# Performance work log

Hardware: AMD Instinct MI355X
Metric: run time of the kernel (lower is better)

The kernel has to match this reference:

```python
import jax, jax.numpy as jnp
import numpy as np

B, N, QD = 2, 2048, 1024
CTX_LEN, TCD = 77, 768
NUM_PROMPT, PD = 64, 1024
HEADS, DIM_HEAD = 8, 64
INNER = HEADS * DIM_HEAD  # 512
SCALE = DIM_HEAD ** -0.5


def setup_inputs() -> dict:
    key = jax.random.key(0)
    ks = jax.random.split(key, 10)
    s = lambda *sh: 1.0 / np.sqrt(sh[0])
    return {
        "x": jax.random.normal(ks[0], (B, N, QD), jnp.float32),
        "context": jax.random.normal(ks[1], (B, CTX_LEN, TCD), jnp.float32),
        "prompt": jax.random.normal(ks[2], (1, NUM_PROMPT, PD), jnp.float32),
        "w_prompt": jax.random.normal(ks[3], (PD, TCD), jnp.float32) * s(PD),
        "w_img": jax.random.normal(ks[4], (QD, TCD), jnp.float32) * s(QD),
        "w_q": jax.random.normal(ks[5], (QD, INNER), jnp.float32) * s(QD),
        "w_k": jax.random.normal(ks[6], (TCD, INNER), jnp.float32) * s(TCD),
        "w_v": jax.random.normal(ks[7], (TCD, INNER), jnp.float32) * s(TCD),
        "w_out": jax.random.normal(ks[8], (INNER, QD), jnp.float32) * s(INNER),
        "b_out": jax.random.normal(ks[9], (QD,), jnp.float32) * 0.01,
    }


def reference(x, context, prompt, w_prompt, w_img, w_q, w_k, w_v, w_out, b_out):
    b, n, _ = x.shape
    # q projection
    q = x @ w_q  # [B, N, INNER]
    # build kv context: [text ; projected prompt ; projected image tokens]
    prompt_ctx = jnp.broadcast_to(prompt @ w_prompt, (b, NUM_PROMPT, TCD))
    img_ctx = x @ w_img  # [B, N, TCD]
    ctx = jnp.concatenate([context, prompt_ctx, img_ctx], axis=1)  # [B, J, TCD]
    k = ctx @ w_k
    v = ctx @ w_v
    # split heads: [B, H, L, D]
    split = lambda t: t.reshape(b, t.shape[1], HEADS, DIM_HEAD).transpose(0, 2, 1, 3)
    qh, kh, vh = split(q), split(k), split(v)
    sim = jnp.einsum("bhid,bhjd->bhij", qh, kh) * SCALE
    attn = jax.nn.softmax(sim, axis=-1)
    out = jnp.einsum("bhij,bhjd->bhid", attn, vh)  # [B, H, N, D]
    out = out.transpose(0, 2, 1, 3).reshape(b, n, INNER)
    return out @ w_out + b_out
```

## Files before the change

kernel.cpp:

```cpp
#include <hip/hip_runtime.h>
#include <hip/hip_bf16.h>
#include <math.h>

#define BB 2
#define NN 2048
#define QD 1024
#define CTX_LEN 77
#define TCD 768
#define NUM_PROMPT 64
#define PD 1024
#define HEADS 8
#define DIM_HEAD 64
#define INNER 512
#define JTOT (CTX_LEN + NUM_PROMPT + NN)
#define SCALE 0.125f
#define SCALEL2 (0.125f * 1.44269504088896f)
#define MTOT (BB * NN)
#define JPAD 2240
#define KVPAD 2304
#define NT_J (JPAD / 64)
#define NT_SPLIT 18

typedef unsigned short u16;
typedef unsigned int u32;
typedef __attribute__((ext_vector_type(8))) short bf16x8;
typedef __attribute__((ext_vector_type(4))) float f32x4;

__device__ __forceinline__ u32 pack_split(float f) {
  u32 u = __builtin_bit_cast(u32, f);
  u32 hi = u & 0xffff0000u;
  float lo = f - __builtin_bit_cast(float, hi);
  u32 ul = __builtin_bit_cast(u32, lo);
  return __builtin_amdgcn_perm(ul, u, 0x07060302u);
}
__device__ __forceinline__ void split2(float f, u16& h, u16& l) {
  u32 u = __builtin_bit_cast(u32, f);
  u32 hm = u & 0xffff0000u;
  float lo = f - __builtin_bit_cast(float, hm);
  h = (u16)(u >> 16);
  l = (u16)(__builtin_bit_cast(u32, lo) >> 16);
}
__device__ __forceinline__ u16 rnd_bf16(float f) {
  u32 u = __builtin_bit_cast(u32, f);
  return (u16)((u + 0x7FFF + ((u >> 16) & 1)) >> 16);
}
__device__ __forceinline__ ushort4 pack4r(const float4& f) {
  ushort4 r;
  r.x = rnd_bf16(f.x); r.y = rnd_bf16(f.y);
  r.z = rnd_bf16(f.z); r.w = rnd_bf16(f.w);
  return r;
}

template <int CTRL>
__device__ __forceinline__ float dpp_f(float x) {
  int i = __builtin_bit_cast(int, x);
  i = __builtin_amdgcn_update_dpp(0, i, CTRL, 0xF, 0xF, false);
  return __builtin_bit_cast(float, i);
}

__device__ __forceinline__ void gload16(const u16* g, u32* l) {
  __builtin_amdgcn_global_load_lds(
      (const __attribute__((address_space(1))) u32*)(const void*)g,
      (__attribute__((address_space(3))) u32*)(void*)l, 16, 0, 0);
}

__global__ __launch_bounds__(256) void pack_planes4(
    const float* __restrict__ s0, u16* __restrict__ d0, int n0,
    const float* __restrict__ s1, u16* __restrict__ d1, int n1,
    const float* __restrict__ ctx, u16* __restrict__ ch, int n2,
    u16* __restrict__ zh, int n3) {
  int i = blockIdx.x * 256 + threadIdx.x;
  if (i < n0) {
    ((ushort4*)d0)[i] = pack4r(((const float4*)s0)[i]);
    return;
  }
  i -= n0;
  if (i < n1) {
    ((ushort4*)d1)[i] = pack4r(((const float4*)s1)[i]);
    return;
  }
  i -= n1;
  if (i < n2) {
    ushort4 rr = pack4r(((const float4*)ctx)[i]);
    int c4 = i % (TCD / 4);
    int rb = i / (TCD / 4);
    int r = rb % CTX_LEN, b = rb / CTX_LEN;
    size_t o = ((size_t)b * JTOT + r) * (TCD / 4) + c4;
    ((ushort4*)ch)[o] = rr;
    return;
  }
  i -= n2;
  if (i >= n3) return;
  int c = i & 7;
  int row = i >> 3;
  int d = row & 511;
  int b = row >> 9;
  uint4 z = {0u, 0u, 0u, 0u};
  *(uint4*)&zh[((size_t)b * INNER + d) * KVPAD + 2176 + c * 8] = z;
}

struct TP6 {
  const float* src[6];
  u16* dh[6];
  u16* dl[6];
  int K[6], N[6];
  int blk0[7];
};

__global__ __launch_bounds__(256) void transpose_pack6(TP6 P) {
  __shared__ u32 T[32][33];
  const int bid = blockIdx.x;
  int s = 0;
#pragma unroll
  for (int k = 1; k < 6; ++k) s += (bid >= P.blk0[k]);
  const int rel = bid - P.blk0[s];
  const int N = P.N[s], K = P.K[s];
  const int nbx = N >> 5;
  const int bx = rel % nbx, by = rel / nbx;
  const float* __restrict__ src = P.src[s];
  u16* __restrict__ dh = P.dh[s];
  u16* __restrict__ dl = P.dl[s];
  const int t = threadIdx.x;
  const int k0 = by * 32, n0 = bx * 32;
#pragma unroll
  for (int i = 0; i < 4; ++i) {
    int e = t + i * 256;
    int kr = e >> 5, nc = e & 31;
    T[kr][nc] = pack_split(src[(size_t)(k0 + kr) * N + n0 + nc]);
  }
  __syncthreads();
#pragma unroll
  for (int i = 0; i < 4; ++i) {
    int e = t + i * 256;
    int nr = e >> 5, kc = e & 31;
    u32 w = T[kc][nr];
    size_t idx = (size_t)(n0 + nr) * K + k0 + kc;
    if (dl) {
      dh[idx] = (u16)(w & 0xffff);
      dl[idx] = (u16)(w >> 16);
    } else {
      dh[idx] = (u16)(w & 0xffff);
    }
  }
}

template <int MODE>
__global__ __launch_bounds__(256) void gemm_mfma(
    const u16* __restrict__ Agh, const u16* __restrict__ Agl,
    const u16* __restrict__ Bgh, const u16* __restrict__ Bgl,
    u16* __restrict__ O1h,
    u16* __restrict__ O2h,
    float* __restrict__ Of, const float* __restrict__ bias,
    int M, int K, int Ntot,
    const u16* __restrict__ A2h, const u16* __restrict__ B2h) {
  constexpr bool ONET = (MODE == 1 || MODE == 2);
  constexpr int ALSZ = ONET ? 4 : 2 * 128 * 16;
  constexpr int BLSZ = ONET ? 4 : 2 * 64 * 16;
  __shared__ __align__(16) u32 Ah_s[2][128 * 16];
  __shared__ __align__(16) u32 Al_s[ALSZ];
  __shared__ __align__(16) u32 Bh_s[2][64 * 16];
  __shared__ __align__(16) u32 Bl_s[BLSZ];

  int bxi = blockIdx.x, byi = blockIdx.y;
  {
    const int GX = gridDim.x;
    const int nwg = GX * gridDim.y;
    const int lid = byi * GX + bxi;
    const int qq = nwg >> 3, rr = nwg & 7;
    const int xcd = lid & 7, pos = lid >> 3;
    const int swz = (xcd < rr ? xcd * (qq + 1) : rr * (qq + 1) + (xcd - rr) * qq) + pos;
    bxi = swz % GX; byi = swz / GX;
  }
  const int bm = byi * 128, bn = bxi * 64;

  const bool pband = (MODE == 1) && (bm >= MTOT);
  if (pband && bn >= TCD) return;

  int b2 = 0, jbase = 0;
  if (MODE == 2) { b2 = (byi >= 18); jbase = (byi - b2 * 18) * 128; }

  const int t = threadIdx.x;
  const int w = t >> 6, lane = t & 63;
  const int m16 = lane & 15, quad = lane >> 4;
  const int wm = w >> 1, wn = w & 1;

  const u16* Abh = Agh; const u16* Abl = Agl;
  const u16* Bbh = Bgh; const u16* Bbl = Bgl;
  int rowlim = M - 1;
  int bmA = bm;
  if (pband) { Abh = A2h; Bbh = B2h; rowlim = NUM_PROMPT - 1; bmA = 0; }

  const int acol = (lane & 3) * 8;
  const int ar0 = 32 * w + (lane >> 2);
  const int ar1 = ar0 + 16;
  int ag0, ag1;
  if (MODE == 2) {
    ag0 = b2 * JTOT + min(jbase + ar0, JTOT - 1);
    ag1 = b2 * JTOT + min(jbase + ar1, JTOT - 1);
  } else {
    ag0 = min(bmA + ar0, rowlim);
    ag1 = min(bmA + ar1, rowlim);
  }
  const u16* a0h = Abh + (size_t)ag0 * K + acol;
  const u16* a1h = Abh + (size_t)ag1 * K + acol;
  const u16* a0l = ONET ? nullptr : Abl + (size_t)ag0 * K + acol;
  const u16* a1l = ONET ? nullptr : Abl + (size_t)ag1 * K + acol;
  const int br = 16 * w + (lane >> 2);
  const u16* b0h = Bbh + (size_t)(bn + br) * K + acol;
  const u16* b0l = ONET ? nullptr : Bbl + (size_t)(bn + br) * K + acol;

  f32x4 acc[4][2];
#pragma unroll
  for (int i = 0; i < 4; ++i)
#pragma unroll
    for (int j = 0; j < 2; ++j) acc[i][j] = (f32x4){0.f, 0.f, 0.f, 0.f};

  for (int k0 = 0; k0 < K; k0 += 64) {
#pragma unroll
    for (int s = 0; s < 2; ++s) {
      const int kc = k0 + s * 32;
      gload16(a0h + kc, &Ah_s[s][(2 * w) * 256]);
      gload16(a1h + kc, &Ah_s[s][(2 * w + 1) * 256]);
      gload16(b0h + kc, &Bh_s[s][w * 256]);
      if constexpr (!ONET) {
        gload16(a0l + kc, &Al_s[s * 2048 + (2 * w) * 256]);
        gload16(a1l + kc, &Al_s[s * 2048 + (2 * w + 1) * 256]);
        gload16(b0l + kc, &Bl_s[s * 1024 + w * 256]);
      }
    }
    __syncthreads();

#pragma unroll
    for (int s = 0; s < 2; ++s) {
      bf16x8 ah[4], al[4], bh[2], bl[2];
#pragma unroll
      for (int mt = 0; mt < 4; ++mt) {
        int off = (wm * 64 + mt * 16 + m16) * 16 + quad * 4;
        ah[mt] = *(const bf16x8*)&Ah_s[s][off];
        if constexpr (!ONET) al[mt] = *(const bf16x8*)&Al_s[s * 2048 + off];
      }
#pragma unroll
      for (int nt = 0; nt < 2; ++nt) {
        int off = (wn * 32 + nt * 16 + m16) * 16 + quad * 4;
        bh[nt] = *(const bf16x8*)&Bh_s[s][off];
        if constexpr (!ONET) bl[nt] = *(const bf16x8*)&Bl_s[s * 1024 + off];
      }
#pragma unroll
      for (int mt = 0; mt < 4; ++mt)
#pragma unroll
        for (int nt = 0; nt < 2; ++nt) {
          acc[mt][nt] = __builtin_amdgcn_mfma_f32_16x16x32_bf16(ah[mt], bh[nt], acc[mt][nt], 0, 0, 0);
          if constexpr (!ONET) {
            acc[mt][nt] = __builtin_amdgcn_mfma_f32_16x16x32_bf16(ah[mt], bl[nt], acc[mt][nt], 0, 0, 0);
            acc[mt][nt] = __builtin_amdgcn_mfma_f32_16x16x32_bf16(al[mt], bh[nt], acc[mt][nt], 0, 0, 0);
          }
        }
    }
    __syncthreads();
  }

  if (MODE == 2 && bn >= INNER) {
    u16* Th = (u16*)Ah_s;
#pragma unroll
    for (int mt = 0; mt < 4; ++mt)
#pragma unroll
      for (int nt = 0; nt < 2; ++nt)
#pragma unroll
        for (int r = 0; r < 4; ++r) {
          int dl = wn * 32 + nt * 16 + m16;
          int jl = wm * 64 + mt * 16 + quad * 4 + r;
          int adr = dl * 128 + ((((jl >> 3) ^ (dl & 15)) << 3) | (jl & 7));
          Th[adr] = rnd_bf16(acc[mt][nt][r]);
        }
    __syncthreads();
#pragma unroll
    for (int i = 0; i < 4; ++i) {
      int chunk = t + i * 256;
      int dl = chunk >> 4, jc = chunk & 15;
      int jg = jbase + jc * 8;
      int lofs = dl * 128 + ((jc ^ (dl & 15)) << 3);
      uint4 vh4 = *(const uint4*)&Th[lofs];
      size_t rowo = ((size_t)b2 * INNER + (bn - INNER) + dl) * KVPAD;
      if (jg + 8 <= JTOT) {
        *(uint4*)&O2h[rowo + jg] = vh4;
      } else if (jg < JTOT) {
        const u16* eh = (const u16*)&vh4;
#pragma unroll
        for (int e = 0; e < 8; ++e)
          if (jg + e < JTOT) O2h[rowo + jg + e] = eh[e];
      }
    }
    return;
  }

#pragma unroll
  for (int mt = 0; mt < 4; ++mt)
#pragma unroll
    for (int nt = 0; nt < 2; ++nt)
#pragma unroll
      for (int r = 0; r < 4; ++r) {
        int gm = bm + wm * 64 + mt * 16 + quad * 4 + r;
        int gn = bn + wn * 32 + nt * 16 + m16;
        float v = acc[mt][nt][r];
        if (MODE == 1) {
          if (pband) {
            int pr = wm * 64 + mt * 16 + quad * 4 + r;
            if (pr < NUM_PROMPT && gn < TCD) {
              u16 rv = rnd_bf16(v);
              O1h[((size_t)CTX_LEN + pr) * TCD + gn] = rv;
              O1h[((size_t)JTOT + CTX_LEN + pr) * TCD + gn] = rv;
            }
          } else if (gn < TCD) {
            size_t row = (size_t)(gm >> 11) * JTOT + 141 + (gm & 2047);
            O1h[row * TCD + gn] = rnd_bf16(v);
          } else {
            O2h[(size_t)gm * INNER + (gn - TCD)] = rnd_bf16(v * SCALEL2);
          }
        } else if (MODE == 2) {
          int jloc = jbase + wm * 64 + mt * 16 + quad * 4 + r;
          O1h[((size_t)b2 * KVPAD + jloc) * INNER + gn] = rnd_bf16(v);
        } else if (MODE == 3) {
          Of[(size_t)gm * QD + gn] = v + bias[gn];
        }
      }
}

__global__ __launch_bounds__(256) void attn_mfma2(
    const u16* __restrict__ qhg,
    const u16* __restrict__ khg,
    const u16* __restrict__ vtg_h,
    float* __restrict__ Opart, float* __restrict__ lsum) {
  __shared__ __align__(16) u16 Kh_s[64 * 64];
  __shared__ __align__(16) u16 Vh_s[64 * 64];
  __shared__ __align__(16) u16 Ph_s[64 * 72];

  const int t = threadIdx.x;
  const int w = t >> 6, lane = t & 63;
  const int m16 = lane & 15, quad = lane >> 4;

  const int id = blockIdx.x;
  const int swz = (id & 7) * 128 + (id >> 3);
  const int jh = swz & 1;
  const int qt = (swz >> 1) & 31;
  const int bh = swz >> 6;
  const int b = bh >> 3, h = bh & 7;
  const int qrow0 = qt * 64;
  const int t0 = jh ? NT_SPLIT : 0;
  const int t1 = jh ? NT_J : NT_SPLIT;

  bf16x8 qh[2];
  {
    size_t qoff = ((size_t)(b * NN + qrow0 + w * 16 + m16)) * INNER + h * 64 + quad * 8;
#pragma unroll
    for (int ks = 0; ks < 2; ++ks)
      qh[ks] = *(const bf16x8*)(qhg + qoff + ks * 32);
  }

  const int sr = lane >> 3;
  const int sc = (lane & 7) ^ sr;
  const int c0 = (w & 1) * 4;
  const u16* gp;
  u32* lp;
  size_t cstr, jstr;
  if (w < 2) {
    gp = khg + ((size_t)b * KVPAD + t0 * 64 + c0 * 8 + sr) * INNER + h * 64 + sc * 8;
    lp = (u32*)Kh_s + c0 * 256;
    cstr = (size_t)8 * INNER;
    jstr = (size_t)64 * INNER;
  } else {
    gp = vtg_h + ((size_t)b * INNER + h * 64 + c0 * 8 + sr) * KVPAD + t0 * 64 + sc * 8;
    lp = (u32*)Vh_s + c0 * 256;
    cstr = (size_t)8 * KVPAD;
    jstr = 64;
  }

  f32x4 O[4] = {{0.f,0.f,0.f,0.f},{0.f,0.f,0.f,0.f},{0.f,0.f,0.f,0.f},{0.f,0.f,0.f,0.f}};
  float lpart[4];
#pragma unroll
  for (int r = 0; r < 4; ++r) lpart[r] = 0.f;

  for (int tile = t0; tile < t1; ++tile) {
    const int j0 = tile * 64;
    __syncthreads();
#pragma unroll
    for (int c = 0; c < 4; ++c) gload16(gp + (size_t)c * cstr, lp + c * 256);
    gp += jstr;
    __syncthreads();

    f32x4 S[4];
    __builtin_amdgcn_s_setprio(1);
#pragma unroll
    for (int jt = 0; jt < 4; ++jt) {
      const int row = jt * 16 + m16;
      f32x4 acc = {0.f, 0.f, 0.f, 0.f};
#pragma unroll
      for (int ks = 0; ks < 2; ++ks) {
        const int cc = row * 64 + (((ks * 4 + quad) ^ (row & 7)) << 3);
        bf16x8 kh = *(const bf16x8*)&Kh_s[cc];
        acc = __builtin_amdgcn_mfma_f32_16x16x32_bf16(qh[ks], kh, acc, 0, 0, 0);
      }
      S[jt] = acc;
    }
    __builtin_amdgcn_s_setprio(0);

    if (j0 + 64 > JTOT) {
#pragma unroll
      for (int jt = 0; jt < 4; ++jt) {
        int jc = j0 + jt * 16 + m16;
        if (jc >= JTOT)
#pragma unroll
          for (int r = 0; r < 4; ++r) S[jt][r] = -INFINITY;
      }
    }

    float pj[4][4];
#pragma unroll
    for (int jt = 0; jt < 4; ++jt)
#pragma unroll
      for (int r = 0; r < 4; ++r) {
        float pv = __builtin_amdgcn_exp2f(S[jt][r] - 8.f);
        pj[jt][r] = pv;
        lpart[r] += pv;
      }

#pragma unroll
    for (int jt = 0; jt < 4; ++jt)
#pragma unroll
      for (int r = 0; r < 4; ++r) {
        int pq = (w * 16 + quad * 4 + r) * 72 + jt * 16 + m16;
        Ph_s[pq] = rnd_bf16(pj[jt][r]);
      }

    bf16x8 ph[2];
#pragma unroll
    for (int ks = 0; ks < 2; ++ks) {
      int po = (w * 16 + m16) * 72 + ks * 32 + quad * 8;
      ph[ks] = *(const bf16x8*)&Ph_s[po];
    }

    __builtin_amdgcn_s_setprio(1);
#pragma unroll
    for (int nt = 0; nt < 4; ++nt) {
      const int row = nt * 16 + m16;
#pragma unroll
      for (int ks = 0; ks < 2; ++ks) {
        const int cc = row * 64 + (((ks * 4 + quad) ^ (row & 7)) << 3);
        bf16x8 vh = *(const bf16x8*)&Vh_s[cc];
        O[nt] = __builtin_amdgcn_mfma_f32_16x16x32_bf16(ph[ks], vh, O[nt], 0, 0, 0);
      }
    }
    __builtin_amdgcn_s_setprio(0);
  }

  float lres[4];
#pragma unroll
  for (int r = 0; r < 4; ++r) {
    float rs = lpart[r];
    rs += dpp_f<0xB1>(rs);
    rs += dpp_f<0x4E>(rs);
    rs += dpp_f<0x124>(rs);
    rs += dpp_f<0x128>(rs);
    lres[r] = rs;
  }
  if (m16 == 0) {
#pragma unroll
    for (int r = 0; r < 4; ++r) {
      size_t row = (size_t)b * NN + qrow0 + w * 16 + quad * 4 + r;
      lsum[((size_t)jh * MTOT + row) * HEADS + h] = lres[r];
    }
  }
#pragma unroll
  for (int nt = 0; nt < 4; ++nt)
#pragma unroll
    for (int r = 0; r < 4; ++r) {
      size_t idx = ((size_t)jh * MTOT + b * NN + qrow0 + w * 16 + quad * 4 + r) * INNER +
                   h * 64 + nt * 16 + m16;
      Opart[idx] = O[nt][r];
    }
}

__global__ __launch_bounds__(256) void combine_attn(
    const float* __restrict__ Opart, const float* __restrict__ lsum,
    u16* __restrict__ aoh, u16* __restrict__ aol) {
  int i = blockIdx.x * 256 + threadIdx.x;
  const int total4 = MTOT * INNER / 4;
  if (i >= total4) return;
  int row = i / (INNER / 4);
  int c4 = (i % (INNER / 4)) * 4;
  int h = c4 >> 6;
  float4 o0 = ((const float4*)Opart)[i];
  float4 o1 = ((const float4*)(Opart + (size_t)MTOT * INNER))[i];
  float l = lsum[(size_t)row * HEADS + h] + lsum[((size_t)MTOT + row) * HEADS + h];
  float inv = 1.f / l;
  float v0 = (o0.x + o1.x) * inv;
  float v1 = (o0.y + o1.y) * inv;
  float v2 = (o0.z + o1.z) * inv;
  float v3 = (o0.w + o1.w) * inv;
  ushort4 hh, ll;
  split2(v0, hh.x, ll.x); split2(v1, hh.y, ll.y);
  split2(v2, hh.z, ll.z); split2(v3, hh.w, ll.w);
  ((ushort4*)aoh)[i] = hh;
  ((ushort4*)aol)[i] = ll;
}

extern "C" void kernel_launch(void* const* d_in, const int* in_sizes, int n_in,
                              void* d_out, int out_size, void* d_ws, size_t ws_size,
                              hipStream_t stream) {
  const float* x        = (const float*)d_in[0];
  const float* context  = (const float*)d_in[1];
  const float* prompt   = (const float*)d_in[2];
  const float* w_prompt = (const float*)d_in[3];
  const float* w_img    = (const float*)d_in[4];
  const float* w_q      = (const float*)d_in[5];
  const float* w_k      = (const float*)d_in[6];
  const float* w_v      = (const float*)d_in[7];
  const float* w_out    = (const float*)d_in[8];
  const float* b_out    = (const float*)d_in[9];
  float* out = (float*)d_out;

  const int M = MTOT;
  const int MJ = BB * JTOT;

  u16* p = (u16*)d_ws;
  const size_t qN = (size_t)M * INNER;
  const size_t ctxN = (size_t)MJ * TCD;
  const size_t kN = (size_t)BB * KVPAD * INNER;
  u16* cth = p; p += ctxN;
  u16* aoh = p; p += qN;   u16* aol = p; p += qN;
  u16* xh  = p; p += (size_t)M * QD;
  u16* prh = p; p += (size_t)NUM_PROMPT * PD;
  u16* WtPh = p; p += (size_t)TCD * PD;
  u16* WtAh = p; p += (size_t)(TCD + INNER) * QD;
  u16* WtBh = p; p += (size_t)(2 * INNER) * TCD;
  u16* WtOh = p; p += (size_t)QD * INNER;          u16* WtOl = p; p += (size_t)QD * INNER;
  u16* qhp = p; p += qN;
  u16* khp = p; p += kN;
  u16* vthp = p; p += kN;
  float* Opart = (float*)p; p += 2 * qN * 2;
  float* lsum  = (float*)p; p += (size_t)2 * MTOT * HEADS * 2;

  const int n4x = M * QD / 4, n4p = NUM_PROMPT * PD / 4;
  const int n4c = BB * CTX_LEN * TCD / 4;
  const int n4z = BB * INNER * 8;
  pack_planes4<<<(n4x + n4p + n4c + n4z + 255) / 256, 256, 0, stream>>>(
      x, xh, n4x, prompt, prh, n4p, context, cth, n4c, vthp, n4z);

  TP6 tp;
  const float* srcs[6] = {w_prompt, w_img, w_q, w_k, w_v, w_out};
  u16* dhs[6] = {WtPh, WtAh, WtAh + (size_t)TCD * QD, WtBh, WtBh + (size_t)INNER * TCD, WtOh};
  u16* dls[6] = {nullptr, nullptr, nullptr, nullptr, nullptr, WtOl};
  int Ks[6] = {PD, QD, QD, TCD, TCD, INNER};
  int Ns[6] = {TCD, TCD, INNER, INNER, INNER, QD};
  int acc_blk = 0;
  for (int i = 0; i < 6; ++i) {
    tp.src[i] = srcs[i]; tp.dh[i] = dhs[i]; tp.dl[i] = dls[i];
    tp.K[i] = Ks[i]; tp.N[i] = Ns[i];
    tp.blk0[i] = acc_blk;
    acc_blk += (Ns[i] / 32) * (Ks[i] / 32);
  }
  tp.blk0[6] = acc_blk;
  transpose_pack6<<<acc_blk, 256, 0, stream>>>(tp);

  gemm_mfma<1><<<dim3((TCD + INNER) / 64, M / 128 + 1), 256, 0, stream>>>(
      xh, nullptr, WtAh, nullptr, cth, qhp, nullptr, nullptr,
      M, QD, TCD + INNER, prh, WtPh);
  gemm_mfma<2><<<dim3((2 * INNER) / 64, 2 * (KVPAD / 128)), 256, 0, stream>>>(
      cth, nullptr, WtBh, nullptr, khp, vthp, nullptr, nullptr,
      MJ, TCD, 2 * INNER, nullptr, nullptr);
  attn_mfma2<<<BB * HEADS * (NN / 64) * 2, 256, 0, stream>>>(
      qhp, khp, vthp, Opart, lsum);
  combine_attn<<<(M * INNER / 4 + 255) / 256, 256, 0, stream>>>(
      Opart, lsum, aoh, aol);
  gemm_mfma<3><<<dim3(QD / 64, M / 128), 256, 0, stream>>>(
      aoh, aol, WtOh, WtOl, nullptr, nullptr, out, b_out,
      M, INNER, QD, nullptr, nullptr);
}
```

Baseline: 195.2 us.

## Compute transposed attention tiles to keep P in registers via bpermute

Swaps the MFMA operand order so S and O are computed transposed, with each lane holding one query row. The probability tile is then packed to bf16 with a hardware pack-convert and rearranged across lanes using ds_bpermute, which removes the LDS round trip through Ph_s and its extra barrier-free stores and loads. Row sums reduce with two cross-lane shuffles instead of DPP chains, and partial outputs are written as float4 vectors. The cost is eight bpermutes per k-step plus selects, in exchange for less LDS traffic and smaller shared memory.

```diff
diff --git a/kernel.cpp b/kernel.cpp
--- a/kernel.cpp
+++ b/kernel.cpp
@@ -48,6 +48,11 @@
   ushort4 r;
   r.x = rnd_bf16(f.x); r.y = rnd_bf16(f.y);
   r.z = rnd_bf16(f.z); r.w = rnd_bf16(f.w);
+  return r;
+}
+__device__ __forceinline__ u32 cvt_pk_bf16(float lo, float hi) {
+  u32 r;
+  asm("v_cvt_pk_bf16_f32 %0, %1, %2" : "=v"(r) : "v"(lo), "v"(hi));
   return r;
 }
 
@@ -332,7 +337,6 @@
     float* __restrict__ Opart, float* __restrict__ lsum) {
   __shared__ __align__(16) u16 Kh_s[64 * 64];
   __shared__ __align__(16) u16 Vh_s[64 * 64];
-  __shared__ __align__(16) u16 Ph_s[64 * 72];
 
   const int t = threadIdx.x;
   const int w = t >> 6, lane = t & 63;
@@ -374,10 +378,12 @@
     jstr = 64;
   }
 
-  f32x4 O[4] = {{0.f,0.f,0.f,0.f},{0.f,0.f,0.f,0.f},{0.f,0.f,0.f,0.f},{0.f,0.f,0.f,0.f}};
-  float lpart[4];
-#pragma unroll
-  for (int r = 0; r < 4; ++r) lpart[r] = 0.f;
+  f32x4 OT[4] = {{0.f,0.f,0.f,0.f},{0.f,0.f,0.f,0.f},{0.f,0.f,0.f,0.f},{0.f,0.f,0.f,0.f}};
+  float lac = 0.f;
+
+  const int addr0 = 4 * (m16 + 16 * ((2 * quad) & 3));
+  const int addr2 = 4 * (m16 + 16 * ((2 * quad + 1) & 3));
+  const bool hi2 = quad >= 2;
 
   for (int tile = t0; tile < t1; ++tile) {
     const int j0 = tile * 64;
@@ -397,7 +403,7 @@
       for (int ks = 0; ks < 2; ++ks) {
         const int cc = row * 64 + (((ks * 4 + quad) ^ (row & 7)) << 3);
         bf16x8 kh = *(const bf16x8*)&Kh_s[cc];
-        acc = __builtin_amdgcn_mfma_f32_16x16x32_bf16(qh[ks], kh, acc, 0, 0, 0);
+        acc = __builtin_amdgcn_mfma_f32_16x16x32_bf16(kh, qh[ks], acc, 0, 0, 0);
       }
       S[jt] = acc;
     }
@@ -406,10 +412,10 @@
     if (j0 + 64 > JTOT) {
 #pragma unroll
       for (int jt = 0; jt < 4; ++jt) {
-        int jc = j0 + jt * 16 + m16;
-        if (jc >= JTOT)
-#pragma unroll
-          for (int r = 0; r < 4; ++r) S[jt][r] = -INFINITY;
+        int jc = j0 + jt * 16 + quad * 4;
+#pragma unroll
+        for (int r = 0; r < 4; ++r)
+          if (jc + r >= JTOT) S[jt][r] = -INFINITY;
       }
     }
 
@@ -420,22 +426,28 @@
       for (int r = 0; r < 4; ++r) {
         float pv = __builtin_amdgcn_exp2f(S[jt][r] - 8.f);
         pj[jt][r] = pv;
-        lpart[r] += pv;
-      }
-
-#pragma unroll
-    for (int jt = 0; jt < 4; ++jt)
-#pragma unroll
-      for (int r = 0; r < 4; ++r) {
-        int pq = (w * 16 + quad * 4 + r) * 72 + jt * 16 + m16;
-        Ph_s[pq] = rnd_bf16(pj[jt][r]);
-      }
-
-    bf16x8 ph[2];
+        lac += pv;
+      }
+
+    u32 pk[4][2];
+#pragma unroll
+    for (int jt = 0; jt < 4; ++jt) {
+      pk[jt][0] = cvt_pk_bf16(pj[jt][0], pj[jt][1]);
+      pk[jt][1] = cvt_pk_bf16(pj[jt][2], pj[jt][3]);
+    }
+    bf16x8 pb[2];
 #pragma unroll
     for (int ks = 0; ks < 2; ++ks) {
-      int po = (w * 16 + m16) * 72 + ks * 32 + quad * 8;
-      ph[ks] = *(const bf16x8*)&Ph_s[po];
+      union { u32 u[4]; bf16x8 v; } B;
+#pragma unroll
+      for (int i = 0; i < 4; ++i) {
+        const int addr = (i < 2) ? addr0 : addr2;
+        const int half = i & 1;
+        u32 vA = (u32)__builtin_amdgcn_ds_bpermute(addr, (int)pk[2 * ks][half]);
+        u32 vB = (u32)__builtin_amdgcn_ds_bpermute(addr, (int)pk[2 * ks + 1][half]);
+        B.u[i] = hi2 ? vB : vA;
+      }
+      pb[ks] = B.v;
     }
 
     __builtin_amdgcn_s_setprio(1);
@@ -446,37 +458,23 @@
       for (int ks = 0; ks < 2; ++ks) {
         const int cc = row * 64 + (((ks * 4 + quad) ^ (row & 7)) << 3);
         bf16x8 vh = *(const bf16x8*)&Vh_s[cc];
-        O[nt] = __builtin_amdgcn_mfma_f32_16x16x32_bf16(ph[ks], vh, O[nt], 0, 0, 0);
+        OT[nt] = __builtin_amdgcn_mfma_f32_16x16x32_bf16(vh, pb[ks], OT[nt], 0, 0, 0);
       }
     }
     __builtin_amdgcn_s_setprio(0);
   }
 
-  float lres[4];
-#pragma unroll
-  for (int r = 0; r < 4; ++r) {
-    float rs = lpart[r];
-    rs += dpp_f<0xB1>(rs);
-    rs += dpp_f<0x4E>(rs);
-    rs += dpp_f<0x124>(rs);
-    rs += dpp_f<0x128>(rs);
-    lres[r] = rs;
-  }
-  if (m16 == 0) {
-#pragma unroll
-    for (int r = 0; r < 4; ++r) {
-      size_t row = (size_t)b * NN + qrow0 + w * 16 + quad * 4 + r;
-      lsum[((size_t)jh * MTOT + row) * HEADS + h] = lres[r];
-    }
-  }
-#pragma unroll
-  for (int nt = 0; nt < 4; ++nt)
-#pragma unroll
-    for (int r = 0; r < 4; ++r) {
-      size_t idx = ((size_t)jh * MTOT + b * NN + qrow0 + w * 16 + quad * 4 + r) * INNER +
-                   h * 64 + nt * 16 + m16;
-      Opart[idx] = O[nt][r];
-    }
+  lac += __shfl_xor(lac, 16, 64);
+  lac += __shfl_xor(lac, 32, 64);
+  const size_t qrow = (size_t)b * NN + qrow0 + w * 16 + m16;
+  if (quad == 0)
+    lsum[((size_t)jh * MTOT + qrow) * HEADS + h] = lac;
+
+#pragma unroll
+  for (int nt = 0; nt < 4; ++nt) {
+    size_t idx = ((size_t)jh * MTOT + qrow) * INNER + h * 64 + nt * 16 + quad * 4;
+    *(float4*)&Opart[idx] = *(const float4*)&OT[nt];
+  }
 }
 
 __global__ __launch_bounds__(256) void combine_attn(
```

Result: no change. 197.9 us (+1.4%).
